# Performance work log

Hardware: AMD Instinct MI355X
Metric: run time of the kernel (lower is better)

Reference implementation:

```python
import jax, jax.numpy as jnp
import numpy as np

NUM_HEADS = 8
EMBED_DIM = 512
EXPAND = 3
RPE_DIM = 512
RPE_LAYERS = 3
B, N = 4, 2048
D1 = (EXPAND * EMBED_DIM) // NUM_HEADS * NUM_HEADS  # 1536
HEAD_DIM = D1 // NUM_HEADS  # 192


def srms(x):
    # SimpleRMSNorm: x / (||x||_2 * d^{-1/2} + eps)
    d = x.shape[-1]
    rms = jnp.linalg.norm(x, axis=-1, keepdims=True) * (d ** -0.5)
    return x / (rms + 1e-8)


def rpe_net(idx, Wp, bp, Wl, bl, Wr, br):
    # idx: (m, 1) relative positions -> (m, h*head_dim)
    h = idx @ Wp.T + bp
    for i in range(Wl.shape[0]):  # fixed small layer count
        h = jax.nn.relu(srms(h)) @ Wl[i].T + bl[i]
    return jax.nn.relu(srms(h)) @ Wr.T + br


def setup_inputs() -> dict:
    key = jax.random.key(0)
    ks = jax.random.split(key, 12)
    s = 0.02
    return {
        "x": jax.random.normal(ks[0], (B, N, EMBED_DIM), jnp.float32),
        "Wu": jax.random.normal(ks[1], (D1, EMBED_DIM), jnp.float32) * s,
        "bu": jnp.zeros((D1,), jnp.float32),
        "Wv": jax.random.normal(ks[2], (D1, EMBED_DIM), jnp.float32) * s,
        "bv": jnp.zeros((D1,), jnp.float32),
        "Wo": jax.random.normal(ks[3], (EMBED_DIM, D1), jnp.float32) * s,
        "bo": jnp.zeros((EMBED_DIM,), jnp.float32),
        "Wp": jax.random.normal(ks[4], (RPE_DIM, 1), jnp.float32) * s,
        "bp": jax.random.normal(ks[5], (RPE_DIM,), jnp.float32) * s,
        "Wl": jax.random.normal(ks[6], (RPE_LAYERS, RPE_DIM, RPE_DIM), jnp.float32) * s,
        "bl": jax.random.normal(ks[7], (RPE_LAYERS, RPE_DIM), jnp.float32) * s,
        "Wr": jax.random.normal(ks[8], (NUM_HEADS * HEAD_DIM, RPE_DIM), jnp.float32) * s,
        "br": jax.random.normal(ks[9], (NUM_HEADS * HEAD_DIM,), jnp.float32) * s,
    }


def reference(x, Wu, bu, Wv, bv, Wo, bo, Wp, bp, Wl, bl, Wr, br):
    b, n, e = x.shape
    d1 = Wu.shape[0]
    hd = d1 // NUM_HEADS
    u = jax.nn.silu(x @ Wu.T + bu)                       # (b, n, d1)
    v = jax.nn.silu(x @ Wv.T + bv)                       # (b, n, d1)
    v = v.reshape(b, n, NUM_HEADS, hd).transpose(0, 2, 1, 3)  # (b, h, n, d)
    # Tno non-causal, par_type=1: indices [0, 1..n-1, 0, -(n-1)..-1]
    pos = jnp.arange(1, n, dtype=x.dtype)
    zero = jnp.zeros((1,), x.dtype)
    idx = jnp.concatenate([zero, pos, zero, -pos[::-1]])[:, None]  # (2n, 1)
    a = rpe_net(idx, Wp, bp, Wl, bl, Wr, br)             # (2n, h*d)
    a = a.reshape(2 * n, NUM_HEADS, hd).transpose(1, 0, 2)  # (h, 2n, d)
    m = 2 * n
    # circular conv of length 2n along sequence, truncate to n
    y = jnp.fft.rfft(v, m, axis=2) * jnp.fft.rfft(a, m, axis=1)[None]
    out = jnp.fft.irfft(y, m, axis=2)[:, :, :n, :]       # (b, h, n, d)
    out = out.transpose(0, 2, 1, 3).reshape(b, n, d1)    # (b, n, d1)
    return (u * out) @ Wo.T + bo
```

## Files before the change

### kernel.cpp

```cpp
#include <hip/hip_runtime.h>

#define N_SEQ 2048
#define M_FFT 4096
#define D1    1536
#define NH    8
#define HD    192
#define ED    512

typedef __bf16 bf16;
typedef __bf16 bf16x4 __attribute__((ext_vector_type(4)));
typedef __bf16 bf16x8 __attribute__((ext_vector_type(8)));
typedef float  floatx4 __attribute__((ext_vector_type(4)));
typedef float  cx __attribute__((ext_vector_type(2)));

enum { MODE_PLAIN = 0, MODE_SILU_UV = 1, MODE_AT = 3, MODE_RPE = 4 };

__device__ __forceinline__ void gload16(const void* g, void* l) {
    __builtin_amdgcn_global_load_lds(
        (const __attribute__((address_space(1))) void*)g,
        (__attribute__((address_space(3))) void*)l, 16, 0, 0);
}

template<int MODE, typename OutT>
__global__ __launch_bounds__(256) void gemm_bf16(
    const bf16* __restrict__ A, const bf16* __restrict__ Bw,
    const float* __restrict__ bias, const float* __restrict__ bias2,
    OutT* __restrict__ C, OutT* __restrict__ C2,
    int M, int Nc, int K,
    const float* __restrict__ scale_in, float* __restrict__ sumsq_out)
{
    __shared__ __align__(16) bf16 As[128 * 32];
    __shared__ __align__(16) bf16 Bs[128 * 32];

    const int tid  = threadIdx.x;
    const int row0 = blockIdx.y * 128;
    const int col0 = blockIdx.x * 128;
    const int wid  = tid >> 6;
    const int lane = tid & 63;
    const int lm   = lane & 15;
    const int lk   = lane >> 4;
    const int wm   = wid >> 1;
    const int wn   = wid & 1;
    const int ldrow  = tid >> 2;
    const int ldcol8 = (tid & 3) * 8;

    floatx4 acc[4][4] = {};

    const bf16* Ag = A  + ((size_t)(row0 + ldrow)) * K + ldcol8;
    const bf16* Bg = Bw + ((size_t)(col0 + ldrow)) * K + ldcol8;
    bf16* AsW = As + (wid * 16) * 32;
    bf16* BsW = Bs + (wid * 16) * 32;

    for (int k0 = 0; k0 < K; k0 += 32) {
        gload16(Ag + k0, AsW);
        gload16(Ag + (size_t)64 * K + k0, AsW + 64 * 32);
        gload16(Bg + k0, BsW);
        gload16(Bg + (size_t)64 * K + k0, BsW + 64 * 32);
        __syncthreads();

        bf16x8 af[4], bfr[4];
        #pragma unroll
        for (int mi = 0; mi < 4; ++mi)
            af[mi] = *(const bf16x8*)&As[(wm * 64 + mi * 16 + lm) * 32 + lk * 8];
        #pragma unroll
        for (int nj = 0; nj < 4; ++nj)
            bfr[nj] = *(const bf16x8*)&Bs[(wn * 64 + nj * 16 + lm) * 32 + lk * 8];
        #pragma unroll
        for (int mi = 0; mi < 4; ++mi)
            #pragma unroll
            for (int nj = 0; nj < 4; ++nj)
                acc[mi][nj] = __builtin_amdgcn_mfma_f32_16x16x32_bf16(
                    af[mi], bfr[nj], acc[mi][nj], 0, 0, 0);
        __syncthreads();
    }

    const float* bs = bias;
    OutT* dst = C;
    int cadj = 0;
    if (MODE == MODE_SILU_UV && col0 >= D1) { bs = bias2; dst = C2; cadj = D1; }

    float bcol[4];
    #pragma unroll
    for (int nj = 0; nj < 4; ++nj)
        bcol[nj] = bs[col0 - cadj + wn * 64 + nj * 16 + lm];

    if (MODE == MODE_RPE) {
        #pragma unroll
        for (int mi = 0; mi < 4; ++mi) {
            #pragma unroll
            for (int r = 0; r < 4; ++r) {
                const int row = row0 + wm * 64 + mi * 16 + lk * 4 + r;
                float sc = 1.0f;
                if (scale_in)
                    sc = 1.0f / (sqrtf(scale_in[row]) * 0.04419417382415922f + 1e-8f);
                float ssq = 0.0f;
                #pragma unroll
                for (int nj = 0; nj < 4; ++nj) {
                    const int col = col0 + wn * 64 + nj * 16 + lm;
                    float val = acc[mi][nj][r] * sc + bcol[nj];
                    ssq += val * val;
                    ((bf16*)C)[(size_t)row * Nc + col] = (bf16)fmaxf(val, 0.0f);
                }
                ssq += __shfl_xor(ssq, 1, 64);
                ssq += __shfl_xor(ssq, 2, 64);
                ssq += __shfl_xor(ssq, 4, 64);
                ssq += __shfl_xor(ssq, 8, 64);
                if (lm == 0) atomicAdd(&sumsq_out[row], ssq);
            }
        }
        return;
    }

    #pragma unroll
    for (int mi = 0; mi < 4; ++mi) {
        const int rbase = row0 + wm * 64 + mi * 16 + lk * 4;
        float sc[4];
        #pragma unroll
        for (int r = 0; r < 4; ++r) {
            sc[r] = 1.0f;
            if (MODE == MODE_AT && scale_in)
                sc[r] = 1.0f / (sqrtf(scale_in[rbase + r]) * 0.04419417382415922f + 1e-8f);
        }
        #pragma unroll
        for (int nj = 0; nj < 4; ++nj) {
            const int col = col0 - cadj + wn * 64 + nj * 16 + lm;
            float vals[4];
            #pragma unroll
            for (int r = 0; r < 4; ++r) {
                float val = acc[mi][nj][r] * sc[r] + bcol[nj];
                if (MODE == MODE_SILU_UV)
                    val = val / (1.0f + __expf(-val));
                vals[r] = val;
            }
            if (MODE == MODE_SILU_UV) {
                int b = rbase >> 11, s = rbase & 2047;
                bf16x4 o;
                #pragma unroll
                for (int r = 0; r < 4; ++r) o[r] = (bf16)vals[r];
                *(bf16x4*)&((bf16*)dst)[((size_t)(b * D1 + col)) * N_SEQ + s] = o;
            } else if (MODE == MODE_AT) {
                float4 o = make_float4(vals[0], vals[1], vals[2], vals[3]);
                *(float4*)&((float*)C)[(size_t)col * M + rbase] = o;
            } else {
                #pragma unroll
                for (int r = 0; r < 4; ++r)
                    C[(size_t)(rbase + r) * Nc + col] = (OutT)vals[r];
            }
        }
    }
}

__global__ __launch_bounds__(256) void f2b_all_kernel(
    const float* __restrict__ x,  const float* __restrict__ s0,
    const float* __restrict__ s1, const float* __restrict__ s2,
    const float* __restrict__ s3, const float* __restrict__ s4,
    const float* __restrict__ Wp, const float* __restrict__ bp,
    bf16* __restrict__ x_bf, bf16* __restrict__ w_bf,
    float* __restrict__ sumsq, bf16* __restrict__ g0,
    float* __restrict__ twd)
{
    const int bid = blockIdx.x;
    const int tid = threadIdx.x;
    __shared__ float red[4];

    if (bid < 7936) {
        const float* src;
        bf16* dst;
        size_t off;
        if (bid < 4096) {
            src = x; dst = x_bf; off = (size_t)bid * 1024;
        } else {
            int t = bid - 4096;
            int seg = t / 768;
            src = seg == 0 ? s0 : seg == 1 ? s1 : seg == 2 ? s2
                : seg == 3 ? s3 : s4;
            dst = w_bf + (size_t)seg * 786432;
            off = (size_t)(t % 768) * 1024;
        }
        size_t i = off + (size_t)tid * 4;
        float4 f = *(const float4*)(src + i);
        union { bf16 h[4]; short4 s; } u4;
        u4.h[0] = (bf16)f.x; u4.h[1] = (bf16)f.y;
        u4.h[2] = (bf16)f.z; u4.h[3] = (bf16)f.w;
        *(short4*)(dst + i) = u4.s;
    } else if (bid < 7948) {
        size_t i = (size_t)(bid - 7936) * 1024 + (size_t)tid * 4;
        *(float4*)(sumsq + i) = make_float4(0.f, 0.f, 0.f, 0.f);
    } else if (bid < 12044) {
        const int j = bid - 7948;
        float idxv = (j < N_SEQ) ? (float)j
                                 : (j == N_SEQ ? 0.0f : (float)(j - 2 * N_SEQ));
        float h1 = idxv * Wp[tid] + bp[tid];
        float h2 = idxv * Wp[tid + 256] + bp[tid + 256];
        float ss = h1 * h1 + h2 * h2;
        #pragma unroll
        for (int off = 32; off > 0; off >>= 1) ss += __shfl_down(ss, off, 64);
        if ((tid & 63) == 0) red[tid >> 6] = ss;
        __syncthreads();
        float tot = red[0] + red[1] + red[2] + red[3];
        float scale = 1.0f / (sqrtf(tot) * 0.04419417382415922f + 1e-8f);
        g0[(size_t)j * ED + tid]       = (bf16)fmaxf(h1 * scale, 0.0f);
        g0[(size_t)j * ED + tid + 256] = (bf16)fmaxf(h2 * scale, 0.0f);
    } else {
        const int idx = (bid - 12044) * 256 + tid;
        const int j = idx >> 4, tau = idx & 15;
        float sA, cA;
        __sincosf(-6.283185307179586f * (float)(j * tau) * (1.0f / 4096.0f),
                  &sA, &cA);
        cx w; w.x = cA; w.y = sA;
        ((cx*)twd)[idx] = w;
    }
}

#define FFT_LDS_SZ 4381

__device__ __forceinline__ int fpad(int i) { return i + (i >> 4) + 2 * (i >> 8); }

__device__ __forceinline__ cx mkcx(float a, float b) { cx r; r.x = a; r.y = b; return r; }
__device__ __forceinline__ cx cmul(cx a, cx b) {
    cx br = mkcx(-b.y, b.x);
    return a.xx * b + a.yy * br;
}
__device__ __forceinline__ cx cmul_cj(cx a, cx b) {
    cx bc = mkcx(b.x, -b.y);
    cx br = mkcx(b.y, b.x);
    return a.xx * bc + a.yy * br;
}
__device__ __forceinline__ cx cneg_i(cx a) { return mkcx(a.y, -a.x); }
__device__ __forceinline__ cx cpos_i(cx a) { return mkcx(-a.y, a.x); }
__host__ __device__ constexpr int brev4(int t) {
    return ((t & 1) << 3) | ((t & 2) << 1) | ((t & 4) >> 1) | ((t & 8) >> 3);
}

#define CC1 0.9238795325112867f
#define SS1 0.3826834323650898f
#define RR2 0.7071067811865476f

template<bool HZ>
__device__ __forceinline__ void fft16_dif_r4(cx x[16]) {
    const cx W1 = mkcx( CC1, -SS1);
    const cx W2 = mkcx( RR2, -RR2);
    const cx W3 = mkcx( SS1, -CC1);
    const cx W6 = mkcx(-RR2, -RR2);
    const cx W9 = mkcx(-CC1,  SS1);
    #pragma unroll
    for (int n = 0; n < 4; ++n) {
        cx A, B, C, D;
        if (HZ) { A = x[n]; C = x[n]; B = x[n + 4]; D = x[n + 4]; }
        else {
            A = x[n] + x[n + 8];      C = x[n] - x[n + 8];
            B = x[n + 4] + x[n + 12]; D = x[n + 4] - x[n + 12];
        }
        cx s = A - B;
        cx nid = cneg_i(D);
        cx m = C + nid;
        cx p = C - nid;
        x[n] = A + B;
        if (n == 0)      { x[4] = s;            x[8]  = m;           x[12] = p; }
        else if (n == 1) { x[5] = cmul(s, W2);  x[9]  = cmul(m, W1); x[13] = cmul(p, W3); }
        else if (n == 2) { x[6] = cneg_i(s);    x[10] = cmul(m, W2); x[14] = cmul(p, W6); }
        else             { x[7] = cmul(s, W6);  x[11] = cmul(m, W3); x[15] = cmul(p, W9); }
    }
    #pragma unroll
    for (int q = 0; q < 16; q += 4) {
        cx a = x[q], b = x[q + 1], c = x[q + 2], d = x[q + 3];
        cx a1 = a + c, c1 = a - c;
        cx b1 = b + d, d1 = cneg_i(b - d);
        x[q]     = a1 + b1;
        x[q + 1] = a1 - b1;
        x[q + 2] = c1 + d1;
        x[q + 3] = c1 - d1;
    }
}

template<bool HALF_OUT>
__device__ __forceinline__ void fft16_dit_inv_r4(cx x[16]) {
    const cx V1 = mkcx( CC1, SS1);
    const cx V2 = mkcx( RR2, RR2);
    const cx V3 = mkcx( SS1, CC1);
    const cx V6 = mkcx(-RR2, RR2);
    #pragma unroll
    for (int q = 0; q < 16; q += 4) {
        cx a = x[q], b = x[q + 1], c = x[q + 2], d = x[q + 3];
        cx a1 = a + b, b1 = a - b;
        cx c1 = c + d, d1 = c - d;
        cx t = cpos_i(d1);
        x[q]     = a1 + c1;
        x[q + 2] = a1 - c1;
        x[q + 1] = b1 + t;
        x[q + 3] = b1 - t;
    }
    #pragma unroll
    for (int n = 0; n < 4; ++n) {
        cx t1, t2;
        if (n == 0)      { t1 = x[4];             t2 = x[12]; }
        else if (n == 1) { t1 = cmul(x[5],  V2);  t2 = cmul(x[13], V2); }
        else if (n == 2) { t1 = cpos_i(x[6]);     t2 = cpos_i(x[14]); }
        else             { t1 = cmul(x[7],  V6);  t2 = cmul(x[15], V6); }
        cx P = x[n] + t1, Q = x[n] - t1;
        cx R = x[n + 8] + t2, S = x[n + 8] - t2;
        cx t, u;
        if (n == 0)      { t = R;            u = S; }
        else if (n == 1) { t = cmul(R, V1);  u = cmul(S, V1); }
        else if (n == 2) { t = cmul(R, V2);  u = cmul(S, V2); }
        else             { t = cmul(R, V3);  u = cmul(S, V3); }
        cx iu = cpos_i(u);
        x[n]     = P + t;
        x[n + 4] = Q + iu;
        if (!HALF_OUT) {
            x[n + 8]  = P - t;
            x[n + 12] = Q - iu;
        }
    }
}

template<bool CONJ>
__device__ __forceinline__ void apply_tw(cx v[16], const cx tw[16]) {
    #pragma unroll
    for (int tau = 1; tau < 16; ++tau) {
        const int q = brev4(tau);
        v[q] = CONJ ? cmul_cj(v[q], tw[tau]) : cmul(v[q], tw[tau]);
    }
}

template<bool CONJ>
__device__ __forceinline__ void apply_tw_lds(cx v[16], const cx* twrow) {
    #pragma unroll
    for (int tau = 1; tau < 16; ++tau) {
        cx w = twrow[tau * 16];
        const int q = brev4(tau);
        v[q] = CONJ ? cmul_cj(v[q], w) : cmul(v[q], w);
    }
}

template<bool HALF_ZERO>
__device__ __forceinline__ void fft4096_fwd_core(
    cx* d, int tid, const cx tw[16], const cx* tw2lds, cx v[16])
{
    {
        fft16_dif_r4<HALF_ZERO>(v);
        apply_tw<false>(v, tw);
        cx* base = d + fpad(tid);
        #pragma unroll
        for (int p = 0; p < 16; ++p) base[274 * p] = v[p];
    }
    __syncthreads();
    {
        cx* base = d + fpad(((tid >> 4) << 8) + (tid & 15));
        #pragma unroll
        for (int t = 0; t < 16; ++t) v[t] = base[17 * t];
        fft16_dif_r4<false>(v);
        apply_tw_lds<false>(v, tw2lds + (tid & 15));
        #pragma unroll
        for (int p = 0; p < 16; ++p) base[17 * p] = v[p];
    }
    __syncthreads();
    {
        cx* base = d + fpad(tid << 4);
        #pragma unroll
        for (int t = 0; t < 16; ++t) v[t] = base[t];
        fft16_dif_r4<false>(v);
        #pragma unroll
        for (int p = 0; p < 16; ++p) base[p] = v[p];
    }
    __syncthreads();
}

__global__ __launch_bounds__(256, 4) void fft_a_kernel(
    const float* a_t, cx* __restrict__ A0s, cx* A1s,
    const cx* __restrict__ Twd)
{
    __shared__ cx data[FFT_LDS_SZ];
    __shared__ cx tw2lds[256];
    const int tid = threadIdx.x;
    const int r = blockIdx.x;

    cx tw[16];
    {
        const cx* Tr1 = Twd + (tid << 4);
        #pragma unroll
        for (int t = 1; t < 16; ++t) tw[t] = Tr1[t];
        tw2lds[(tid >> 4) * 16 + (tid & 15)] = Twd[(tid & 15) * 256 + (tid >> 4)];
    }

    const float* r0 = a_t + (size_t)(2 * r) * M_FFT;
    const float* r1 = r0 + M_FFT;
    cx v[16];
    #pragma unroll
    for (int t = 0; t < 16; ++t)
        v[t] = mkcx(r0[tid + 256 * t], r1[tid + 256 * t]);

    fft4096_fwd_core<false>(data, tid, tw, tw2lds, v);

    const float c = 0.25f / 4096.0f;
    cx* A0row = A0s + (size_t)r * 4096;
    cx* A1row = A1s + (size_t)r * 4096;
    if (tid == 0) {
        #pragma unroll
        for (int i = 0; i < 16; ++i) {
            const int p2 = (i < 2) ? i : (i ^ ((1 << (31 - __clz(i))) - 1));
            cx Wk = data[fpad(i)];
            cx Wm = data[fpad(p2)];
            cx cjWm = mkcx(Wm.x, -Wm.y);
            A0row[i] = c * (Wk + cjWm);
            A1row[i] = c * cneg_i(Wk - cjWm);
        }
    } else {
        const int base = tid << 4;
        const int mask = (1 << (31 - __clz(base))) - 1;
        const cx* zb  = data + fpad(base);
        const cx* zb2 = data + fpad((base ^ mask) - 15);
        #pragma unroll
        for (int i = 0; i < 16; ++i) {
            cx Wk = zb[i];
            cx Wm = zb2[15 - i];
            cx cjWm = mkcx(Wm.x, -Wm.y);
            A0row[base + i] = c * (Wk + cjWm);
            A1row[base + i] = c * cneg_i(Wk - cjWm);
        }
    }
}

__global__ __launch_bounds__(256, 4) void fft_conv_kernel(
    const bf16* __restrict__ v_t, const cx* __restrict__ A0s,
    const cx* __restrict__ A1s, const bf16* __restrict__ u_t,
    bf16* __restrict__ gated_t, const cx* __restrict__ Twd)
{
    __shared__ cx data[FFT_LDS_SZ];
    __shared__ cx tw2lds[256];
    const int tid = threadIdx.x;
    const int bx = blockIdx.x;
    const int xcd  = bx & 7;
    const int slot = bx >> 3;
    const int b    = slot & 3;
    const int r    = (slot >> 2) * 8 + xcd;
    const int ch = 2 * r;

    cx tw[16];
    {
        const cx* Tr1 = Twd + (tid << 4);
        #pragma unroll
        for (int t = 1; t < 16; ++t) tw[t] = Tr1[t];
        tw2lds[(tid >> 4) * 16 + (tid & 15)] = Twd[(tid & 15) * 256 + (tid >> 4)];
    }

    const bf16* z0 = v_t + ((size_t)(b * D1 + ch)) * N_SEQ;
    const bf16* z1 = z0 + N_SEQ;
    cx v[16];
    #pragma unroll
    for (int t = 0; t < 8; ++t)
        v[t] = mkcx((float)z0[tid + 256 * t], (float)z1[tid + 256 * t]);

    fft4096_fwd_core<true>(data, tid, tw, tw2lds, v);

    const cx* A0row = A0s + (size_t)r * 4096;
    const cx* A1row = A1s + (size_t)r * 4096;
    const int pbase = tid << 4;
    {
        float4 a0pf[8], a1pf[8];
        {
            const float4* A0p = (const float4*)(A0row + pbase);
            const float4* A1p = (const float4*)(A1row + pbase);
            #pragma unroll
            for (int i = 0; i < 8; ++i) { a0pf[i] = A0p[i]; a1pf[i] = A1p[i]; }
        }
        auto pf = [](const float4* p, int i) -> cx {
            return (i & 1) ? mkcx(p[i >> 1].z, p[i >> 1].w)
                           : mkcx(p[i >> 1].x, p[i >> 1].y);
        };
        if (tid == 0) {
            #pragma unroll
            for (int i = 0; i < 16; ++i) {
                const int p2 = (i < 2) ? i : (i ^ ((1 << (31 - __clz(i))) - 1));
                cx Zk = data[fpad(i)];
                cx Zm = data[fpad(p2)];
                cx cjZm = mkcx(Zm.x, -Zm.y);
                cx V0 = Zk + cjZm;
                cx V1 = cneg_i(Zk - cjZm);
                v[i] = cmul(V0, pf(a0pf, i)) + cpos_i(cmul(V1, pf(a1pf, i)));
            }
        } else {
            const int mask = (1 << (31 - __clz(pbase))) - 1;
            const cx* zb  = data + fpad(pbase);
            const cx* zb2 = data + fpad((pbase ^ mask) - 15);
            #pragma unroll
            for (int i = 0; i < 16; ++i) {
                cx Zk = zb[i];
                cx Zm = zb2[15 - i];
                cx cjZm = mkcx(Zm.x, -Zm.y);
                cx V0 = Zk + cjZm;
                cx V1 = cneg_i(Zk - cjZm);
                v[i] = cmul(V0, pf(a0pf, i)) + cpos_i(cmul(V1, pf(a1pf, i)));
            }
        }
        __syncthreads();
        fft16_dit_inv_r4<false>(v);
        cx* base = data + fpad(pbase);
        #pragma unroll
        for (int i = 0; i < 16; ++i) base[i] = v[i];
    }
    __syncthreads();
    {
        cx* base = data + fpad(((tid >> 4) << 8) + (tid & 15));
        #pragma unroll
        for (int p = 0; p < 16; ++p) v[p] = base[17 * p];
        apply_tw_lds<true>(v, tw2lds + (tid & 15));
        fft16_dit_inv_r4<false>(v);
        #pragma unroll
        for (int t = 0; t < 16; ++t) base[17 * t] = v[t];
    }
    __syncthreads();
    {
        cx* base = data + fpad(tid);
        #pragma unroll
        for (int p = 0; p < 16; ++p) v[p] = base[274 * p];
        apply_tw<true>(v, tw);
        fft16_dit_inv_r4<true>(v);
        #pragma unroll
        for (int t = 0; t < 8; ++t) base[274 * t] = v[t];
    }
    __syncthreads();

    const bf16* u0 = u_t + ((size_t)(b * D1 + ch)) * N_SEQ;
    const bf16* u1 = u0 + N_SEQ;
    bf16* g0 = gated_t + ((size_t)(b * D1 + ch)) * N_SEQ;
    bf16* g1 = g0 + N_SEQ;
    {
        const int t = tid * 8;
        const cx* base = data + fpad(t);
        bf16x8 ua = *(const bf16x8*)(u0 + t);
        bf16x8 ub = *(const bf16x8*)(u1 + t);
        bf16x8 oa, ob;
        #pragma unroll
        for (int i = 0; i < 8; ++i) {
            cx y = base[i];
            oa[i] = (bf16)(y.x * (float)ua[i]);
            ob[i] = (bf16)(y.y * (float)ub[i]);
        }
        *(bf16x8*)(g0 + t) = oa;
        *(bf16x8*)(g1 + t) = ob;
    }
}

__global__ __launch_bounds__(256) void transpose_cs_kernel(
    const bf16* __restrict__ in, bf16* __restrict__ outp)
{
    __shared__ bf16 tile[64 * 68];
    const int c0 = blockIdx.x * 64;
    const int m0 = blockIdx.y * 64;
    const int b  = m0 >> 11;
    const int s0 = m0 & 2047;
    const int tid = threadIdx.x;
    const int cl = tid >> 4;
    const int sc = (tid & 15) * 4;
    #pragma unroll
    for (int p = 0; p < 4; ++p) {
        int c = p * 16 + cl;
        bf16x4 v = *(const bf16x4*)&in[((size_t)(b * D1 + c0 + c)) * N_SEQ + s0 + sc];
        *(bf16x4*)&tile[c * 68 + sc] = v;
    }
    __syncthreads();
    const int sl = tid >> 4;
    const int cc = (tid & 15) * 4;
    #pragma unroll
    for (int p = 0; p < 4; ++p) {
        int s = p * 16 + sl;
        bf16x4 o;
        #pragma unroll
        for (int j = 0; j < 4; ++j) o[j] = tile[(cc + j) * 68 + s];
        *(bf16x4*)&outp[((size_t)(m0 + s)) * D1 + c0 + cc] = o;
    }
}

extern "C" void kernel_launch(void* const* d_in, const int* in_sizes, int n_in,
                              void* d_out, int out_size, void* d_ws, size_t ws_size,
                              hipStream_t stream)
{
    const float* x  = (const float*)d_in[0];
    const float* Wu = (const float*)d_in[1];
    const float* bu = (const float*)d_in[2];
    const float* Wv = (const float*)d_in[3];
    const float* bv = (const float*)d_in[4];
    const float* Wo = (const float*)d_in[5];
    const float* bo = (const float*)d_in[6];
    const float* Wp = (const float*)d_in[7];
    const float* bp = (const float*)d_in[8];
    const float* Wl = (const float*)d_in[9];
    const float* bl = (const float*)d_in[10];
    const float* Wr = (const float*)d_in[11];
    const float* br = (const float*)d_in[12];
    float* out = (float*)d_out;

    float* ws      = (float*)d_ws;
    float* a_t     = ws;
    float* A0spec  = a_t   + 6291456;
    float* sumsq   = A0spec + 6291456;
    float* twd     = sumsq + 12288;
    bf16*  bfws    = (bf16*)(twd + 8192);
    bf16*  x_bf    = bfws;
    bf16*  w_bf    = x_bf    + 4194304;
    bf16*  Wuv_bf  = w_bf;
    bf16*  Wo_bf   = w_bf    + 2 * 786432;
    bf16*  Wl_bf   = Wo_bf   + 786432;
    bf16*  Wr_bf   = Wl_bf   + 786432;
    bf16*  gA      = Wr_bf   + 786432;
    bf16*  gB      = gA      + 2097152;
    bf16*  u_t     = gB      + 2097152;
    bf16*  v_t     = u_t     + 12582912;
    bf16*  gated_t = v_t     + 12582912;
    bf16*  gated   = gated_t + 12582912;

    dim3 blk(256);

    f2b_all_kernel<<<4096 + 5 * 768 + 12 + 4096 + 16, blk, 0, stream>>>(
        x, Wu, Wv, Wo, Wl, Wr, Wp, bp, x_bf, w_bf, sumsq, gA, twd);

    gemm_bf16<MODE_SILU_UV, bf16><<<dim3(24, 64), blk, 0, stream>>>(
        x_bf, Wuv_bf, bu, bv, u_t, v_t, 8192, 2 * D1, ED, nullptr, nullptr);

    bf16* gin = gA;
    bf16* gout = gB;
    for (int i = 0; i < 3; ++i) {
        const float* sin_p = (i == 0) ? nullptr : sumsq + (size_t)(i - 1) * 4096;
        gemm_bf16<MODE_RPE, bf16><<<dim3(4, 32), blk, 0, stream>>>(
            gin, Wl_bf + (size_t)i * ED * ED, bl + (size_t)i * ED, nullptr,
            gout, nullptr, 4096, ED, ED, sin_p, sumsq + (size_t)i * 4096);
        bf16* t = gin; gin = gout; gout = t;
    }
    gemm_bf16<MODE_AT, float><<<dim3(12, 32), blk, 0, stream>>>(
        gin, Wr_bf, br, nullptr, a_t, nullptr, 4096, D1, ED,
        sumsq + 2 * 4096, nullptr);

    fft_a_kernel<<<768, blk, 0, stream>>>(
        a_t, (cx*)A0spec, (cx*)a_t, (const cx*)twd);
    fft_conv_kernel<<<3072, blk, 0, stream>>>(
        v_t, (const cx*)A0spec, (const cx*)a_t, u_t, gated_t, (const cx*)twd);

    transpose_cs_kernel<<<dim3(24, 128), blk, 0, stream>>>(gated_t, gated);

    gemm_bf16<MODE_PLAIN, float><<<dim3(4, 64), blk, 0, stream>>>(
        gated, Wo_bf, bo, nullptr, out, nullptr, 8192, ED, D1,
        nullptr, nullptr);
}
```

Before: 370.2 us.

## Double-buffer LDS tiles in bf16 GEMM to overlap global loads with MFMA

Splits the shared-memory A/B tiles into two buffers and prefetches the next K-slice via global_load_lds while computing on the current one. This is meant to hide global-to-LDS load latency behind the MFMA work instead of stalling on a barrier every iteration. It doubles LDS use per block, which may lower occupancy. The loop assumes the number of K tiles is even.

Measured after the change: 357.2 us. 3.5% less time.

```diff
diff --git a/kernel.cpp b/kernel.cpp
--- a/kernel.cpp
+++ b/kernel.cpp
@@ -29,8 +29,8 @@
     int M, int Nc, int K,
     const float* __restrict__ scale_in, float* __restrict__ sumsq_out)
 {
-    __shared__ __align__(16) bf16 As[128 * 32];
-    __shared__ __align__(16) bf16 Bs[128 * 32];
+    __shared__ __align__(16) bf16 As[2][128 * 32];
+    __shared__ __align__(16) bf16 Bs[2][128 * 32];
 
     const int tid  = threadIdx.x;
     const int row0 = blockIdx.y * 128;
@@ -48,29 +48,39 @@
 
     const bf16* Ag = A  + ((size_t)(row0 + ldrow)) * K + ldcol8;
     const bf16* Bg = Bw + ((size_t)(col0 + ldrow)) * K + ldcol8;
-    bf16* AsW = As + (wid * 16) * 32;
-    bf16* BsW = Bs + (wid * 16) * 32;
-
-    for (int k0 = 0; k0 < K; k0 += 32) {
-        gload16(Ag + k0, AsW);
-        gload16(Ag + (size_t)64 * K + k0, AsW + 64 * 32);
-        gload16(Bg + k0, BsW);
-        gload16(Bg + (size_t)64 * K + k0, BsW + 64 * 32);
-        __syncthreads();
-
+    const int woff = (wid * 16) * 32;
+
+    auto stage = [&](int k0, int buf) {
+        gload16(Ag + k0, &As[buf][woff]);
+        gload16(Ag + (size_t)64 * K + k0, &As[buf][woff + 64 * 32]);
+        gload16(Bg + k0, &Bs[buf][woff]);
+        gload16(Bg + (size_t)64 * K + k0, &Bs[buf][woff + 64 * 32]);
+    };
+    auto compute = [&](int buf) {
         bf16x8 af[4], bfr[4];
         #pragma unroll
         for (int mi = 0; mi < 4; ++mi)
-            af[mi] = *(const bf16x8*)&As[(wm * 64 + mi * 16 + lm) * 32 + lk * 8];
+            af[mi] = *(const bf16x8*)&As[buf][(wm * 64 + mi * 16 + lm) * 32 + lk * 8];
         #pragma unroll
         for (int nj = 0; nj < 4; ++nj)
-            bfr[nj] = *(const bf16x8*)&Bs[(wn * 64 + nj * 16 + lm) * 32 + lk * 8];
+            bfr[nj] = *(const bf16x8*)&Bs[buf][(wn * 64 + nj * 16 + lm) * 32 + lk * 8];
         #pragma unroll
         for (int mi = 0; mi < 4; ++mi)
             #pragma unroll
             for (int nj = 0; nj < 4; ++nj)
                 acc[mi][nj] = __builtin_amdgcn_mfma_f32_16x16x32_bf16(
                     af[mi], bfr[nj], acc[mi][nj], 0, 0, 0);
+    };
+
+    const int nt = K >> 5;
+    stage(0, 0);
+    __syncthreads();
+    for (int t = 0; t < nt; t += 2) {
+        stage((t + 1) << 5, 1);
+        compute(0);
+        __syncthreads();
+        if (t + 2 < nt) stage((t + 2) << 5, 0);
+        compute(1);
         __syncthreads();
     }
 
```
